# Performance work log

Hardware: AMD Instinct MI355X
Metric: run time of the kernel (lower is better)

Reference implementation:

```python
import jax, jax.numpy as jnp
import numpy as np

N_DRUG = 50000
N_GENE = 50000
E = 600000
D_IN = 128
D_HID = 64
D_EMB = 32


def setup_inputs() -> dict:
    key = jax.random.key(0)
    ks = jax.random.split(key, 32)
    inp = {}
    inp['x_drug'] = jax.random.normal(ks[0], (N_DRUG, D_IN), jnp.float32)
    inp['x_gene'] = jax.random.normal(ks[1], (N_GENE, D_IN), jnp.float32)
    # per-etype edge lists (src,dst)
    inp['dd_src'] = jax.random.randint(ks[2], (E,), 0, N_DRUG)
    inp['dd_dst'] = jax.random.randint(ks[3], (E,), 0, N_DRUG)
    inp['dg_src'] = jax.random.randint(ks[4], (E,), 0, N_DRUG)
    inp['dg_dst'] = jax.random.randint(ks[5], (E,), 0, N_GENE)
    inp['gd_src'] = jax.random.randint(ks[6], (E,), 0, N_GENE)
    inp['gd_dst'] = jax.random.randint(ks[7], (E,), 0, N_DRUG)
    inp['gg_src'] = jax.random.randint(ks[8], (E,), 0, N_GENE)
    inp['gg_dst'] = jax.random.randint(ks[9], (E,), 0, N_GENE)
    # layer-1 per-relation weights (in -> hidden) and per-ntype biases
    s1 = 1.0 / np.sqrt(D_IN)
    inp['W1_dd'] = jax.random.normal(ks[10], (D_IN, D_HID), jnp.float32) * s1
    inp['W1_dg'] = jax.random.normal(ks[11], (D_IN, D_HID), jnp.float32) * s1
    inp['W1_gd'] = jax.random.normal(ks[12], (D_IN, D_HID), jnp.float32) * s1
    inp['W1_gg'] = jax.random.normal(ks[13], (D_IN, D_HID), jnp.float32) * s1
    inp['b1_drug'] = jnp.zeros((D_HID,), jnp.float32)
    inp['b1_gene'] = jnp.zeros((D_HID,), jnp.float32)
    # layer-2 per-relation weights (hidden -> embed) and per-ntype biases
    s2 = 1.0 / np.sqrt(D_HID)
    inp['W2_dd'] = jax.random.normal(ks[14], (D_HID, D_EMB), jnp.float32) * s2
    inp['W2_dg'] = jax.random.normal(ks[15], (D_HID, D_EMB), jnp.float32) * s2
    inp['W2_gd'] = jax.random.normal(ks[16], (D_HID, D_EMB), jnp.float32) * s2
    inp['W2_gg'] = jax.random.normal(ks[17], (D_HID, D_EMB), jnp.float32) * s2
    inp['b2_drug'] = jnp.zeros((D_EMB,), jnp.float32)
    inp['b2_gene'] = jnp.zeros((D_EMB,), jnp.float32)
    return inp


def _rel_mean(x_src, W, src, dst, n_dst):
    # transform-then-gather (efficient when out_dim <= in_dim), segment-mean over dst
    m = (x_src @ W)[src]                                  # [E, out]
    s = jax.ops.segment_sum(m, dst, num_segments=n_dst)   # [n_dst, out]
    deg = jax.ops.segment_sum(jnp.ones((src.shape[0],), m.dtype), dst, num_segments=n_dst)
    return s / jnp.maximum(deg, 1.0)[:, None]


def _rgcn_layer(xd, xg, Wdd, Wdg, Wgd, Wgg, bd, bg,
                dd_src, dd_dst, dg_src, dg_dst, gd_src, gd_dst, gg_src, gg_dst, act):
    hd = (_rel_mean(xd, Wdd, dd_src, dd_dst, N_DRUG)
          + _rel_mean(xg, Wgd, gd_src, gd_dst, N_DRUG) + bd)
    hg = (_rel_mean(xd, Wdg, dg_src, dg_dst, N_GENE)
          + _rel_mean(xg, Wgg, gg_src, gg_dst, N_GENE) + bg)
    if act:
        hd = jax.nn.relu(hd)
        hg = jax.nn.relu(hg)
    return hd, hg


def reference(x_drug, x_gene, dd_src, dd_dst, dg_src, dg_dst, gd_src, gd_dst,
              gg_src, gg_dst, W1_dd, W1_dg, W1_gd, W1_gg, b1_drug, b1_gene,
              W2_dd, W2_dg, W2_gd, W2_gg, b2_drug, b2_gene):
    hd, hg = _rgcn_layer(x_drug, x_gene, W1_dd, W1_dg, W1_gd, W1_gg, b1_drug, b1_gene,
                         dd_src, dd_dst, dg_src, dg_dst, gd_src, gd_dst, gg_src, gg_dst, True)
    hd, hg = _rgcn_layer(hd, hg, W2_dd, W2_dg, W2_gd, W2_gg, b2_drug, b2_gene,
                         dd_src, dd_dst, dg_src, dg_dst, gd_src, gd_dst, gg_src, gg_dst, False)
    # concatenate per-ntype embeddings: rows [0:N_DRUG]=drug, [N_DRUG:]=gene
    return jnp.concatenate([hd, hg], axis=0)
```

## Files before the change

### kernel.cpp

```cpp
#include <hip/hip_runtime.h>
#include <hip/hip_bf16.h>

#define N_NODE 50000
#define NEDGE  600000
#define NRANGE 128
#define RSZ    391
#define CAPB   6144
#define CHUNK  4096
#define NBLK1  147

typedef __hip_bfloat16 bf16;
struct __attribute__((aligned(8))) bh4 { bf16 a, b, c, d; };
typedef __attribute__((ext_vector_type(8))) short short8;
typedef __attribute__((ext_vector_type(4))) float floatx4;

__device__ __forceinline__ short f2s(float f) {
    bf16 t = __float2bfloat16(f);
    return *(short*)&t;
}


__global__ __launch_bounds__(256) void k_part(
    const int* __restrict__ d0, const int* __restrict__ s0,
    const int* __restrict__ d1, const int* __restrict__ s1,
    const int* __restrict__ d2, const int* __restrict__ s2,
    const int* __restrict__ d3, const int* __restrict__ s3,
    int* __restrict__ gcur, unsigned* __restrict__ gpart)
{
    __shared__ int hcur[NRANGE];
    __shared__ int delta[NRANGE];
    __shared__ int sc[256];
    __shared__ unsigned buf[CHUNK];
    int bid = blockIdx.x;
    int rel = bid / NBLK1;
    int c   = bid - rel * NBLK1;
    int tid = threadIdx.x;
    const int* dp = rel == 0 ? d0 : rel == 1 ? d1 : rel == 2 ? d2 : d3;
    const int* sp = rel == 0 ? s0 : rel == 1 ? s1 : rel == 2 ? s2 : s3;
    int e0 = c * CHUNK;
    int e1 = min(e0 + CHUNK, NEDGE);
    int cnt_chunk = e1 - e0;

    if (tid < NRANGE) hcur[tid] = 0;
    __syncthreads();
    for (int e = e0 + tid; e < e1; e += 256)
        atomicAdd(&hcur[dp[e] / RSZ], 1);
    __syncthreads();
    int v = (tid < NRANGE) ? hcur[tid] : 0;
    sc[tid] = v;
    __syncthreads();
    for (int d = 1; d < NRANGE; d <<= 1) {
        int t = (tid >= d && tid < NRANGE) ? sc[tid - d] : 0;
        __syncthreads();
        sc[tid] += t;
        __syncthreads();
    }
    if (tid < NRANGE) {
        int start = sc[tid] - v;
        int bg    = rel * NRANGE + tid;
        int resv  = atomicAdd(&gcur[bg], v);
        delta[tid] = bg * CAPB + resv - start;
        hcur[tid]  = start;
    }
    __syncthreads();
    for (int e = e0 + tid; e < e1; e += 256) {
        int d = dp[e];
        int b = d / RSZ;
        int p = atomicAdd(&hcur[b], 1);
        buf[p] = ((unsigned)b << 25) | ((unsigned)(d - b * RSZ) << 16) | (unsigned)sp[e];
    }
    __syncthreads();
    for (int i = tid; i < cnt_chunk; i += 256) {
        unsigned key = buf[i];
        gpart[delta[key >> 25] + i] = key;
    }
}

__global__ __launch_bounds__(512) void k_base(
    const int* __restrict__ gcur, int* __restrict__ base_rel)
{
    __shared__ int sc[512];
    int t = threadIdx.x;
    int v = gcur[t];
    sc[t] = v;
    __syncthreads();
    int loc = t & (NRANGE - 1);
    for (int d = 1; d < NRANGE; d <<= 1) {
        int x = (loc >= d) ? sc[t - d] : 0;
        __syncthreads();
        sc[t] += x;
        __syncthreads();
    }
    base_rel[t] = sc[t] - v;
}

__global__ __launch_bounds__(256) void k_csr(
    const unsigned* __restrict__ gpart, const int* __restrict__ gcnt,
    const int* __restrict__ base_rel, int* __restrict__ off, int* __restrict__ edges)
{
    __shared__ int cur[RSZ];
    __shared__ unsigned short stg[CAPB];
    __shared__ int sc[256];
    int bid = blockIdx.x;
    int rel = bid >> 7, r = bid & (NRANGE - 1);
    int tid = threadIdx.x;
    int range0 = r * RSZ;
    int RS = min(RSZ, N_NODE - range0);
    if (RS < 0) RS = 0;
    int count = gcnt[bid];
    int base  = base_rel[bid];
    size_t slot0 = (size_t)bid * CAPB;

    for (int i = tid; i < RSZ; i += 256) cur[i] = 0;
    __syncthreads();
    for (int i = tid; i < count; i += 256)
        atomicAdd(&cur[(gpart[slot0 + i] >> 16) & 0x1FF], 1);
    __syncthreads();
    int vloc[2]; int run = 0;
#pragma unroll
    for (int j = 0; j < 2; j++) {
        int idx = tid * 2 + j;
        int x = (idx < RSZ) ? cur[idx] : 0;
        vloc[j] = x; run += x;
    }
    sc[tid] = run;
    __syncthreads();
    for (int d = 1; d < 256; d <<= 1) {
        int t = (tid >= d) ? sc[tid - d] : 0;
        __syncthreads();
        sc[tid] += t;
        __syncthreads();
    }
    int excl = sc[tid] - run;
    run = excl;
#pragma unroll
    for (int j = 0; j < 2; j++) {
        int idx = tid * 2 + j;
        if (idx < RSZ) { int x = vloc[j]; cur[idx] = run; run += x; }
    }
    __syncthreads();
    for (int i = tid; i < RS; i += 256)
        off[rel * (N_NODE + 1) + range0 + i] = base + cur[i];
    if (r == NRANGE - 1 && tid == 0) off[rel * (N_NODE + 1) + N_NODE] = NEDGE;
    __syncthreads();
    for (int i = tid; i < count; i += 256) {
        unsigned key = gpart[slot0 + i];
        int p = atomicAdd(&cur[(key >> 16) & 0x1FF], 1);
        stg[p] = (unsigned short)(key & 0xFFFFu);
    }
    __syncthreads();
    for (int i = tid; i < count; i += 256)
        edges[rel * NEDGE + base + i] = (int)stg[i];
}

template <int K, int NOUT, bool AFP32>
__global__ __launch_bounds__(256) void k_gemm_pair(
    const void* __restrict__ X0, const void* __restrict__ X1,
    const float* __restrict__ Wa0, const float* __restrict__ Wb0,
    const float* __restrict__ Wa1, const float* __restrict__ Wb1,
    bf16* __restrict__ out0, bf16* __restrict__ out1, int M)
{
    constexpr int NB  = NOUT / 16;
    constexpr int KC  = K / 32;
    constexpr int NH  = NOUT / 2;
    constexpr int NBL = (NB == 8) ? 3 : 2;
    __shared__ short Wl[KC * NB * 512];

    int sel = blockIdx.y;
    const void*  X  = sel ? X1 : X0;
    const float* Wa = sel ? Wa1 : Wa0;
    const float* Wb = sel ? Wb1 : Wb0;
    bf16*        out = sel ? out1 : out0;

    int tid = threadIdx.x;
    for (int i = tid; i < KC * NB * 512; i += 256) {
        int j  = i & 7;
        int n  = (i >> 3) & 15;
        int q  = (i >> 7) & 3;
        int nb = (i >> 9) & (NB - 1);
        int kc = i >> (9 + NBL);
        int k  = kc * 32 + q * 8 + j;
        int c  = nb * 16 + n;
        float w = (c < NH) ? Wa[k * NH + c] : Wb[k * NH + (c - NH)];
        Wl[i] = f2s(w);
    }
    __syncthreads();

    int lane = tid & 63, wv = tid >> 6;
    int q = lane >> 4, lidx = lane & 15;
    int row0 = blockIdx.x * 64 + wv * 16;
    int rowA = min(row0 + lidx, M - 1);

    floatx4 acc[NB];
#pragma unroll
    for (int nb = 0; nb < NB; nb++) acc[nb] = (floatx4){0.f, 0.f, 0.f, 0.f};

#pragma unroll
    for (int kc = 0; kc < KC; kc++) {
        short8 a;
        if constexpr (AFP32) {
            const float* Xf = (const float*)X + (size_t)rowA * K + kc * 32 + q * 8;
            float4 f0 = *(const float4*)Xf;
            float4 f1 = *(const float4*)(Xf + 4);
            a[0] = f2s(f0.x); a[1] = f2s(f0.y); a[2] = f2s(f0.z); a[3] = f2s(f0.w);
            a[4] = f2s(f1.x); a[5] = f2s(f1.y); a[6] = f2s(f1.z); a[7] = f2s(f1.w);
        } else {
            a = *(const short8*)((const short*)X + (size_t)rowA * K + kc * 32 + q * 8);
        }
#pragma unroll
        for (int nb = 0; nb < NB; nb++) {
            short8 b = *(const short8*)&Wl[((kc * NB + nb) * 64 + lane) * 8];
            acc[nb] = __builtin_amdgcn_mfma_f32_16x16x32_bf16(a, b, acc[nb], 0, 0, 0);
        }
    }
#pragma unroll
    for (int nb = 0; nb < NB; nb++) {
#pragma unroll
        for (int r = 0; r < 4; r++) {
            int row = row0 + q * 4 + r;
            if (row < M)
                out[(size_t)row * NOUT + nb * 16 + lidx] = __float2bfloat16(acc[nb][r]);
        }
    }
}

__device__ __forceinline__ void seg_sum64u(
    const unsigned short* __restrict__ mb, int ldm,
    int beg, int end, const int* __restrict__ edges,
    int lane, int lgrp, const unsigned short* base, float s[4])
{
    for (int e = beg; e < end; e += 64) {
        int nb = min(64, end - e);
        int eidx = (lane < nb) ? edges[e + lane] : 0;
        int full = nb & ~7;
        int j = 0;
        for (; j < full; j += 8) {
            int sa = __shfl(eidx, j + lgrp);
            int sb = __shfl(eidx, j + 4 + lgrp);
            uint2 wa = *(const uint2*)(base + (size_t)sa * ldm);
            uint2 wb = *(const uint2*)(base + (size_t)sb * ldm);
            s[0] += __uint_as_float(wa.x << 16);
            s[1] += __uint_as_float(wa.x & 0xFFFF0000u);
            s[2] += __uint_as_float(wa.y << 16);
            s[3] += __uint_as_float(wa.y & 0xFFFF0000u);
            s[0] += __uint_as_float(wb.x << 16);
            s[1] += __uint_as_float(wb.x & 0xFFFF0000u);
            s[2] += __uint_as_float(wb.y << 16);
            s[3] += __uint_as_float(wb.y & 0xFFFF0000u);
        }
        for (; j < nb; j += 4) {
            int sa = __shfl(eidx, j + lgrp);
            float vm = (j + lgrp < nb) ? 1.f : 0.f;
            uint2 w = *(const uint2*)(base + (size_t)sa * ldm);
            s[0] += vm * __uint_as_float(w.x << 16);
            s[1] += vm * __uint_as_float(w.x & 0xFFFF0000u);
            s[2] += vm * __uint_as_float(w.y << 16);
            s[3] += vm * __uint_as_float(w.y & 0xFFFF0000u);
        }
    }
}

__global__ __launch_bounds__(256) void k_gather64x2(
    const bf16* __restrict__ m1, const bf16* __restrict__ m2,
    const int* __restrict__ offA0, const int* __restrict__ eA0,
    const int* __restrict__ offB0, const int* __restrict__ eB0,
    const float* __restrict__ bias0, bf16* __restrict__ out0,
    const int* __restrict__ offA1, const int* __restrict__ eA1,
    const int* __restrict__ offB1, const int* __restrict__ eB1,
    const float* __restrict__ bias1, bf16* __restrict__ out1)
{
    int gw   = (blockIdx.x * 256 + threadIdx.x) >> 6;
    int lane = threadIdx.x & 63;
    int half = (gw >= N_NODE);
    int wid  = gw - (half ? N_NODE : 0);
    const int* offA = half ? offA1 : offA0;
    const int* eA   = half ? eA1   : eA0;
    const int* offB = half ? offB1 : offB0;
    const int* eB   = half ? eB1   : eB0;
    const float* bias = half ? bias1 : bias0;
    bf16* out = half ? out1 : out0;
    int col = half ? 64 : 0;

    int lgrp = lane >> 4, lidx = lane & 15;
    const unsigned short* mb1 = (const unsigned short*)m1;
    const unsigned short* mb2 = (const unsigned short*)m2;
    const unsigned short* base1 = mb1 + col + lidx * 4;
    const unsigned short* base2 = mb2 + col + lidx * 4;

    int begA = offA[wid], endA = offA[wid + 1];
    int begB = offB[wid], endB = offB[wid + 1];
    float sA[4] = {0.f, 0.f, 0.f, 0.f}, sB[4] = {0.f, 0.f, 0.f, 0.f};
    seg_sum64u(mb1, 128, begA, endA, eA, lane, lgrp, base1, sA);
    seg_sum64u(mb2, 128, begB, endB, eB, lane, lgrp, base2, sB);
#pragma unroll
    for (int k = 0; k < 4; k++) {
        sA[k] += __shfl_xor(sA[k], 16); sA[k] += __shfl_xor(sA[k], 32);
        sB[k] += __shfl_xor(sB[k], 16); sB[k] += __shfl_xor(sB[k], 32);
    }
    if (lane < 16) {
        float ia = 1.f / (float)max(endA - begA, 1);
        float ib = 1.f / (float)max(endB - begB, 1);
        float h0 = fmaxf(sA[0] * ia + sB[0] * ib + bias[lidx * 4 + 0], 0.f);
        float h1 = fmaxf(sA[1] * ia + sB[1] * ib + bias[lidx * 4 + 1], 0.f);
        float h2 = fmaxf(sA[2] * ia + sB[2] * ib + bias[lidx * 4 + 2], 0.f);
        float h3 = fmaxf(sA[3] * ia + sB[3] * ib + bias[lidx * 4 + 3], 0.f);
        bh4 v = { __float2bfloat16(h0), __float2bfloat16(h1),
                  __float2bfloat16(h2), __float2bfloat16(h3) };
        *(bh4*)(out + (size_t)wid * 64 + lidx * 4) = v;
    }
}

__device__ __forceinline__ void seg_sum32u(
    int beg, int end, const int* __restrict__ edges,
    int lane, int lgrp, int ldm, const unsigned short* base, float s[4])
{
    for (int e = beg; e < end; e += 64) {
        int nb = min(64, end - e);
        int eidx = (lane < nb) ? edges[e + lane] : 0;
        int full = nb & ~15;
        int j = 0;
        for (; j < full; j += 16) {
            int sa = __shfl(eidx, j + lgrp);
            int sb = __shfl(eidx, j + 8 + lgrp);
            uint2 wa = *(const uint2*)(base + (size_t)sa * ldm);
            uint2 wb = *(const uint2*)(base + (size_t)sb * ldm);
            s[0] += __uint_as_float(wa.x << 16);
            s[1] += __uint_as_float(wa.x & 0xFFFF0000u);
            s[2] += __uint_as_float(wa.y << 16);
            s[3] += __uint_as_float(wa.y & 0xFFFF0000u);
            s[0] += __uint_as_float(wb.x << 16);
            s[1] += __uint_as_float(wb.x & 0xFFFF0000u);
            s[2] += __uint_as_float(wb.y << 16);
            s[3] += __uint_as_float(wb.y & 0xFFFF0000u);
        }
        for (; j < nb; j += 8) {
            int sa = __shfl(eidx, j + lgrp);
            float vm = (j + lgrp < nb) ? 1.f : 0.f;
            uint2 w = *(const uint2*)(base + (size_t)sa * ldm);
            s[0] += vm * __uint_as_float(w.x << 16);
            s[1] += vm * __uint_as_float(w.x & 0xFFFF0000u);
            s[2] += vm * __uint_as_float(w.y << 16);
            s[3] += vm * __uint_as_float(w.y & 0xFFFF0000u);
        }
    }
}

__global__ __launch_bounds__(256) void k_gather32x2(
    const bf16* __restrict__ m1, const bf16* __restrict__ m2,
    const int* __restrict__ offA0, const int* __restrict__ eA0,
    const int* __restrict__ offB0, const int* __restrict__ eB0,
    const float* __restrict__ bias0, float* __restrict__ out0,
    const int* __restrict__ offA1, const int* __restrict__ eA1,
    const int* __restrict__ offB1, const int* __restrict__ eB1,
    const float* __restrict__ bias1, float* __restrict__ out1)
{
    int gw   = (blockIdx.x * 256 + threadIdx.x) >> 6;
    int lane = threadIdx.x & 63;
    int half = (gw >= N_NODE);
    int wid  = gw - (half ? N_NODE : 0);
    const int* offA = half ? offA1 : offA0;
    const int* eA   = half ? eA1   : eA0;
    const int* offB = half ? offB1 : offB0;
    const int* eB   = half ? eB1   : eB0;
    const float* bias = half ? bias1 : bias0;
    float* out = half ? out1 : out0;
    int col = half ? 32 : 0;

    int lgrp = lane >> 3, lidx = lane & 7;
    const unsigned short* base1 = (const unsigned short*)m1 + col + lidx * 4;
    const unsigned short* base2 = (const unsigned short*)m2 + col + lidx * 4;

    int begA = offA[wid], endA = offA[wid + 1];
    int begB = offB[wid], endB = offB[wid + 1];
    float sA[4] = {0.f, 0.f, 0.f, 0.f}, sB[4] = {0.f, 0.f, 0.f, 0.f};
    seg_sum32u(begA, endA, eA, lane, lgrp, 64, base1, sA);
    seg_sum32u(begB, endB, eB, lane, lgrp, 64, base2, sB);
#pragma unroll
    for (int k = 0; k < 4; k++) {
        sA[k] += __shfl_xor(sA[k], 8); sA[k] += __shfl_xor(sA[k], 16); sA[k] += __shfl_xor(sA[k], 32);
        sB[k] += __shfl_xor(sB[k], 8); sB[k] += __shfl_xor(sB[k], 16); sB[k] += __shfl_xor(sB[k], 32);
    }
    if (lane < 8) {
        float ia = 1.f / (float)max(endA - begA, 1);
        float ib = 1.f / (float)max(endB - begB, 1);
        float4 v;
        v.x = sA[0] * ia + sB[0] * ib + bias[lidx * 4 + 0];
        v.y = sA[1] * ia + sB[1] * ib + bias[lidx * 4 + 1];
        v.z = sA[2] * ia + sB[2] * ib + bias[lidx * 4 + 2];
        v.w = sA[3] * ia + sB[3] * ib + bias[lidx * 4 + 3];
        *(float4*)(out + (size_t)wid * 32 + lidx * 4) = v;
    }
}

extern "C" void kernel_launch(void* const* d_in, const int* in_sizes, int n_in,
                              void* d_out, int out_size, void* d_ws, size_t ws_size,
                              hipStream_t stream)
{
    const float* xd = (const float*)d_in[0];
    const float* xg = (const float*)d_in[1];
    const int* dd_src = (const int*)d_in[2];  const int* dd_dst = (const int*)d_in[3];
    const int* dg_src = (const int*)d_in[4];  const int* dg_dst = (const int*)d_in[5];
    const int* gd_src = (const int*)d_in[6];  const int* gd_dst = (const int*)d_in[7];
    const int* gg_src = (const int*)d_in[8];  const int* gg_dst = (const int*)d_in[9];
    const float* W1dd = (const float*)d_in[10];
    const float* W1dg = (const float*)d_in[11];
    const float* W1gd = (const float*)d_in[12];
    const float* W1gg = (const float*)d_in[13];
    const float* b1d  = (const float*)d_in[14];
    const float* b1g  = (const float*)d_in[15];
    const float* W2dd = (const float*)d_in[16];
    const float* W2dg = (const float*)d_in[17];
    const float* W2gd = (const float*)d_in[18];
    const float* W2gg = (const float*)d_in[19];
    const float* b2d  = (const float*)d_in[20];
    const float* b2g  = (const float*)d_in[21];
    float* out = (float*)d_out;

    int* gcur     = (int*)d_ws;
    int* base_rel = gcur + 512;
    int* off      = base_rel + 512;
    int* edges    = off + 4 * (N_NODE + 1);
    bf16* md1     = (bf16*)(edges + 4 * NEDGE);
    bf16* mg1     = md1 + (size_t)N_NODE * 128;
    bf16* hd      = mg1 + (size_t)N_NODE * 128;
    bf16* hg      = hd + (size_t)N_NODE * 64;
    bf16* md2     = md1;
    bf16* mg2     = mg1;
    unsigned* gpart = (unsigned*)md1;

    hipMemsetAsync(gcur, 0, 512 * sizeof(int), stream);
    k_part<<<4 * NBLK1, 256, 0, stream>>>(
        dd_dst, dd_src, gd_dst, gd_src, dg_dst, dg_src, gg_dst, gg_src, gcur, gpart);
    k_base<<<1, 512, 0, stream>>>(gcur, base_rel);
    k_csr<<<512, 256, 0, stream>>>(gpart, gcur, base_rel, off, edges);

    const int* off_dd = off + 0 * (N_NODE + 1);
    const int* off_gd = off + 1 * (N_NODE + 1);
    const int* off_dg = off + 2 * (N_NODE + 1);
    const int* off_gg = off + 3 * (N_NODE + 1);
    const int* e_dd = edges + 0 * NEDGE;
    const int* e_gd = edges + 1 * NEDGE;
    const int* e_dg = edges + 2 * NEDGE;
    const int* e_gg = edges + 3 * NEDGE;

    dim3 gemm_grid((N_NODE + 63) / 64, 2);
    int gather_grid = 2 * N_NODE / 4;

    k_gemm_pair<128, 128, true><<<gemm_grid, 256, 0, stream>>>(
        xd, xg, W1dd, W1dg, W1gd, W1gg, md1, mg1, N_NODE);
    k_gather64x2<<<gather_grid, 256, 0, stream>>>(
        md1, mg1,
        off_dd, e_dd, off_gd, e_gd, b1d, hd,
        off_dg, e_dg, off_gg, e_gg, b1g, hg);

    k_gemm_pair<64, 64, false><<<gemm_grid, 256, 0, stream>>>(
        hd, hg, W2dd, W2dg, W2gd, W2gg, md2, mg2, N_NODE);
    k_gather32x2<<<gather_grid, 256, 0, stream>>>(
        md2, mg2,
        off_dd, e_dd, off_gd, e_gd, b2d, out,
        off_dg, e_dg, off_gg, e_gg, b2g, out + (size_t)N_NODE * 32);
}
```

Measured before the change: 357.6 us.

## Split gathers into per-relation column-sliced tasks with separate combine kernels

Replaces each fused two-relation gather kernel with a task kernel that processes one relation and one 32-column slice per block. Partial means go to a workspace buffer, and a separate elementwise combine kernel adds bias and applies ReLU. Blocks are interleaved by task index so the gathered rows for a given relation and slice stay cache-resident, which is meant to improve locality of the random gathers. In exchange it adds two extra launches and writes and rereads the intermediate partials, with bf16 rounding of the layer-1 partials before they are summed.

```diff
diff --git a/kernel.cpp b/kernel.cpp
--- a/kernel.cpp
+++ b/kernel.cpp
@@ -8,6 +8,7 @@
 #define CAPB   6144
 #define CHUNK  4096
 #define NBLK1  147
+#define SP1    (N_NODE * 32)
 
 typedef __hip_bfloat16 bf16;
 struct __attribute__((aligned(8))) bh4 { bf16 a, b, c, d; };
@@ -224,172 +225,172 @@
     }
 }
 
-__device__ __forceinline__ void seg_sum64u(
-    const unsigned short* __restrict__ mb, int ldm,
-    int beg, int end, const int* __restrict__ edges,
-    int lane, int lgrp, const unsigned short* base, float s[4])
-{
+__global__ __launch_bounds__(256) void k_gtask1(
+    const bf16* __restrict__ md1, const bf16* __restrict__ mg1,
+    const int* __restrict__ off, const int* __restrict__ edges,
+    bf16* __restrict__ p1)
+{
+    int b = blockIdx.x;
+    int t = b & 7;
+    int wv = threadIdx.x >> 6, lane = threadIdx.x & 63;
+    int node = (b >> 3) * 4 + wv;
+    if (node >= N_NODE) return;
+    int r = t >> 1, c = t & 1;
+    const bf16* M = (r == 0 || r == 2) ? md1 : mg1;
+    int col0 = (r < 2 ? 0 : 64) + c * 32;
+    const int* offr = off + r * (N_NODE + 1);
+    const int* er   = edges + r * NEDGE;
+    int beg = offr[node], end = offr[node + 1];
+    int lgrp = lane >> 3, lidx = lane & 7;
+    const unsigned* base = (const unsigned*)M + (col0 >> 1) + lidx * 2;
+    float s0 = 0.f, s1 = 0.f, s2 = 0.f, s3 = 0.f;
     for (int e = beg; e < end; e += 64) {
         int nb = min(64, end - e);
-        int eidx = (lane < nb) ? edges[e + lane] : 0;
-        int full = nb & ~7;
-        int j = 0;
-        for (; j < full; j += 8) {
-            int sa = __shfl(eidx, j + lgrp);
-            int sb = __shfl(eidx, j + 4 + lgrp);
-            uint2 wa = *(const uint2*)(base + (size_t)sa * ldm);
-            uint2 wb = *(const uint2*)(base + (size_t)sb * ldm);
-            s[0] += __uint_as_float(wa.x << 16);
-            s[1] += __uint_as_float(wa.x & 0xFFFF0000u);
-            s[2] += __uint_as_float(wa.y << 16);
-            s[3] += __uint_as_float(wa.y & 0xFFFF0000u);
-            s[0] += __uint_as_float(wb.x << 16);
-            s[1] += __uint_as_float(wb.x & 0xFFFF0000u);
-            s[2] += __uint_as_float(wb.y << 16);
-            s[3] += __uint_as_float(wb.y & 0xFFFF0000u);
-        }
-        for (; j < nb; j += 4) {
-            int sa = __shfl(eidx, j + lgrp);
-            float vm = (j + lgrp < nb) ? 1.f : 0.f;
-            uint2 w = *(const uint2*)(base + (size_t)sa * ldm);
-            s[0] += vm * __uint_as_float(w.x << 16);
-            s[1] += vm * __uint_as_float(w.x & 0xFFFF0000u);
-            s[2] += vm * __uint_as_float(w.y << 16);
-            s[3] += vm * __uint_as_float(w.y & 0xFFFF0000u);
-        }
-    }
-}
-
-__global__ __launch_bounds__(256) void k_gather64x2(
-    const bf16* __restrict__ m1, const bf16* __restrict__ m2,
-    const int* __restrict__ offA0, const int* __restrict__ eA0,
-    const int* __restrict__ offB0, const int* __restrict__ eB0,
-    const float* __restrict__ bias0, bf16* __restrict__ out0,
-    const int* __restrict__ offA1, const int* __restrict__ eA1,
-    const int* __restrict__ offB1, const int* __restrict__ eB1,
-    const float* __restrict__ bias1, bf16* __restrict__ out1)
-{
-    int gw   = (blockIdx.x * 256 + threadIdx.x) >> 6;
-    int lane = threadIdx.x & 63;
-    int half = (gw >= N_NODE);
-    int wid  = gw - (half ? N_NODE : 0);
-    const int* offA = half ? offA1 : offA0;
-    const int* eA   = half ? eA1   : eA0;
-    const int* offB = half ? offB1 : offB0;
-    const int* eB   = half ? eB1   : eB0;
-    const float* bias = half ? bias1 : bias0;
-    bf16* out = half ? out1 : out0;
-    int col = half ? 64 : 0;
-
-    int lgrp = lane >> 4, lidx = lane & 15;
-    const unsigned short* mb1 = (const unsigned short*)m1;
-    const unsigned short* mb2 = (const unsigned short*)m2;
-    const unsigned short* base1 = mb1 + col + lidx * 4;
-    const unsigned short* base2 = mb2 + col + lidx * 4;
-
-    int begA = offA[wid], endA = offA[wid + 1];
-    int begB = offB[wid], endB = offB[wid + 1];
-    float sA[4] = {0.f, 0.f, 0.f, 0.f}, sB[4] = {0.f, 0.f, 0.f, 0.f};
-    seg_sum64u(mb1, 128, begA, endA, eA, lane, lgrp, base1, sA);
-    seg_sum64u(mb2, 128, begB, endB, eB, lane, lgrp, base2, sB);
-#pragma unroll
-    for (int k = 0; k < 4; k++) {
-        sA[k] += __shfl_xor(sA[k], 16); sA[k] += __shfl_xor(sA[k], 32);
-        sB[k] += __shfl_xor(sB[k], 16); sB[k] += __shfl_xor(sB[k], 32);
-    }
-    if (lane < 16) {
-        float ia = 1.f / (float)max(endA - begA, 1);
-        float ib = 1.f / (float)max(endB - begB, 1);
-        float h0 = fmaxf(sA[0] * ia + sB[0] * ib + bias[lidx * 4 + 0], 0.f);
-        float h1 = fmaxf(sA[1] * ia + sB[1] * ib + bias[lidx * 4 + 1], 0.f);
-        float h2 = fmaxf(sA[2] * ia + sB[2] * ib + bias[lidx * 4 + 2], 0.f);
-        float h3 = fmaxf(sA[3] * ia + sB[3] * ib + bias[lidx * 4 + 3], 0.f);
-        bh4 v = { __float2bfloat16(h0), __float2bfloat16(h1),
-                  __float2bfloat16(h2), __float2bfloat16(h3) };
-        *(bh4*)(out + (size_t)wid * 64 + lidx * 4) = v;
-    }
-}
-
-__device__ __forceinline__ void seg_sum32u(
-    int beg, int end, const int* __restrict__ edges,
-    int lane, int lgrp, int ldm, const unsigned short* base, float s[4])
-{
-    for (int e = beg; e < end; e += 64) {
-        int nb = min(64, end - e);
-        int eidx = (lane < nb) ? edges[e + lane] : 0;
+        int eidx = (lane < nb) ? er[e + lane] : 0;
         int full = nb & ~15;
         int j = 0;
         for (; j < full; j += 16) {
             int sa = __shfl(eidx, j + lgrp);
             int sb = __shfl(eidx, j + 8 + lgrp);
-            uint2 wa = *(const uint2*)(base + (size_t)sa * ldm);
-            uint2 wb = *(const uint2*)(base + (size_t)sb * ldm);
-            s[0] += __uint_as_float(wa.x << 16);
-            s[1] += __uint_as_float(wa.x & 0xFFFF0000u);
-            s[2] += __uint_as_float(wa.y << 16);
-            s[3] += __uint_as_float(wa.y & 0xFFFF0000u);
-            s[0] += __uint_as_float(wb.x << 16);
-            s[1] += __uint_as_float(wb.x & 0xFFFF0000u);
-            s[2] += __uint_as_float(wb.y << 16);
-            s[3] += __uint_as_float(wb.y & 0xFFFF0000u);
+            uint2 wa = *(const uint2*)(base + (size_t)sa * 64);
+            uint2 wb = *(const uint2*)(base + (size_t)sb * 64);
+            s0 += __uint_as_float(wa.x << 16);
+            s1 += __uint_as_float(wa.x & 0xFFFF0000u);
+            s2 += __uint_as_float(wa.y << 16);
+            s3 += __uint_as_float(wa.y & 0xFFFF0000u);
+            s0 += __uint_as_float(wb.x << 16);
+            s1 += __uint_as_float(wb.x & 0xFFFF0000u);
+            s2 += __uint_as_float(wb.y << 16);
+            s3 += __uint_as_float(wb.y & 0xFFFF0000u);
         }
         for (; j < nb; j += 8) {
             int sa = __shfl(eidx, j + lgrp);
             float vm = (j + lgrp < nb) ? 1.f : 0.f;
-            uint2 w = *(const uint2*)(base + (size_t)sa * ldm);
-            s[0] += vm * __uint_as_float(w.x << 16);
-            s[1] += vm * __uint_as_float(w.x & 0xFFFF0000u);
-            s[2] += vm * __uint_as_float(w.y << 16);
-            s[3] += vm * __uint_as_float(w.y & 0xFFFF0000u);
-        }
-    }
-}
-
-__global__ __launch_bounds__(256) void k_gather32x2(
-    const bf16* __restrict__ m1, const bf16* __restrict__ m2,
-    const int* __restrict__ offA0, const int* __restrict__ eA0,
-    const int* __restrict__ offB0, const int* __restrict__ eB0,
-    const float* __restrict__ bias0, float* __restrict__ out0,
-    const int* __restrict__ offA1, const int* __restrict__ eA1,
-    const int* __restrict__ offB1, const int* __restrict__ eB1,
-    const float* __restrict__ bias1, float* __restrict__ out1)
-{
-    int gw   = (blockIdx.x * 256 + threadIdx.x) >> 6;
-    int lane = threadIdx.x & 63;
-    int half = (gw >= N_NODE);
-    int wid  = gw - (half ? N_NODE : 0);
-    const int* offA = half ? offA1 : offA0;
-    const int* eA   = half ? eA1   : eA0;
-    const int* offB = half ? offB1 : offB0;
-    const int* eB   = half ? eB1   : eB0;
-    const float* bias = half ? bias1 : bias0;
-    float* out = half ? out1 : out0;
-    int col = half ? 32 : 0;
-
+            uint2 w = *(const uint2*)(base + (size_t)sa * 64);
+            s0 += vm * __uint_as_float(w.x << 16);
+            s1 += vm * __uint_as_float(w.x & 0xFFFF0000u);
+            s2 += vm * __uint_as_float(w.y << 16);
+            s3 += vm * __uint_as_float(w.y & 0xFFFF0000u);
+        }
+    }
+    s0 += __shfl_xor(s0, 8); s0 += __shfl_xor(s0, 16); s0 += __shfl_xor(s0, 32);
+    s1 += __shfl_xor(s1, 8); s1 += __shfl_xor(s1, 16); s1 += __shfl_xor(s1, 32);
+    s2 += __shfl_xor(s2, 8); s2 += __shfl_xor(s2, 16); s2 += __shfl_xor(s2, 32);
+    s3 += __shfl_xor(s3, 8); s3 += __shfl_xor(s3, 16); s3 += __shfl_xor(s3, 32);
+    if (lane < 8) {
+        float inv = 1.f / (float)max(end - beg, 1);
+        bh4 v = { __float2bfloat16(s0 * inv), __float2bfloat16(s1 * inv),
+                  __float2bfloat16(s2 * inv), __float2bfloat16(s3 * inv) };
+        *(bh4*)(p1 + (size_t)t * SP1 + (size_t)node * 32 + lidx * 4) = v;
+    }
+}
+
+__global__ __launch_bounds__(256) void k_combine1(
+    const bf16* __restrict__ p1, const float* __restrict__ b1d,
+    const float* __restrict__ b1g, bf16* __restrict__ hd, bf16* __restrict__ hg)
+{
+    int id = blockIdx.x * 256 + threadIdx.x;
+    if (id >= 2 * N_NODE * 16) return;
+    int half = id >= N_NODE * 16;
+    int rem = id - half * N_NODE * 16;
+    int n = rem >> 4, u = rem & 15;
+    int f0 = u * 4, ch = u >> 3, fi = f0 & 31;
+    const unsigned short* pa = (const unsigned short*)p1
+        + ((size_t)((half ? 4 : 0) + ch)) * SP1 + (size_t)n * 32 + fi;
+    const unsigned short* pb = (const unsigned short*)p1
+        + ((size_t)((half ? 6 : 2) + ch)) * SP1 + (size_t)n * 32 + fi;
+    uint2 wa = *(const uint2*)pa;
+    uint2 wb = *(const uint2*)pb;
+    const float* bias = (half ? b1g : b1d) + f0;
+    float h0 = fmaxf(__uint_as_float(wa.x << 16)          + __uint_as_float(wb.x << 16)          + bias[0], 0.f);
+    float h1 = fmaxf(__uint_as_float(wa.x & 0xFFFF0000u)  + __uint_as_float(wb.x & 0xFFFF0000u)  + bias[1], 0.f);
+    float h2 = fmaxf(__uint_as_float(wa.y << 16)          + __uint_as_float(wb.y << 16)          + bias[2], 0.f);
+    float h3 = fmaxf(__uint_as_float(wa.y & 0xFFFF0000u)  + __uint_as_float(wb.y & 0xFFFF0000u)  + bias[3], 0.f);
+    bf16* h = half ? hg : hd;
+    bh4 v = { __float2bfloat16(h0), __float2bfloat16(h1),
+              __float2bfloat16(h2), __float2bfloat16(h3) };
+    *(bh4*)(h + (size_t)n * 64 + f0) = v;
+}
+
+__global__ __launch_bounds__(256) void k_gtask2(
+    const bf16* __restrict__ md2, const bf16* __restrict__ mg2,
+    const int* __restrict__ off, const int* __restrict__ edges,
+    float* __restrict__ p2)
+{
+    int b = blockIdx.x;
+    int t = b & 7;
+    int wv = threadIdx.x >> 6, lane = threadIdx.x & 63;
+    int r = t >> 1, nh = t & 1;
+    int node = nh * (N_NODE / 2) + (b >> 3) * 4 + wv;
+    int nend = nh * (N_NODE / 2) + N_NODE / 2;
+    if (node >= nend) return;
+    const bf16* M = (r == 0 || r == 2) ? md2 : mg2;
+    int col0 = (r < 2) ? 0 : 32;
+    const int* offr = off + r * (N_NODE + 1);
+    const int* er   = edges + r * NEDGE;
+    int beg = offr[node], end = offr[node + 1];
     int lgrp = lane >> 3, lidx = lane & 7;
-    const unsigned short* base1 = (const unsigned short*)m1 + col + lidx * 4;
-    const unsigned short* base2 = (const unsigned short*)m2 + col + lidx * 4;
-
-    int begA = offA[wid], endA = offA[wid + 1];
-    int begB = offB[wid], endB = offB[wid + 1];
-    float sA[4] = {0.f, 0.f, 0.f, 0.f}, sB[4] = {0.f, 0.f, 0.f, 0.f};
-    seg_sum32u(begA, endA, eA, lane, lgrp, 64, base1, sA);
-    seg_sum32u(begB, endB, eB, lane, lgrp, 64, base2, sB);
-#pragma unroll
-    for (int k = 0; k < 4; k++) {
-        sA[k] += __shfl_xor(sA[k], 8); sA[k] += __shfl_xor(sA[k], 16); sA[k] += __shfl_xor(sA[k], 32);
-        sB[k] += __shfl_xor(sB[k], 8); sB[k] += __shfl_xor(sB[k], 16); sB[k] += __shfl_xor(sB[k], 32);
-    }
+    const unsigned* base = (const unsigned*)M + (col0 >> 1) + lidx * 2;
+    float s0 = 0.f, s1 = 0.f, s2 = 0.f, s3 = 0.f;
+    for (int e = beg; e < end; e += 64) {
+        int nb = min(64, end - e);
+        int eidx = (lane < nb) ? er[e + lane] : 0;
+        int full = nb & ~15;
+        int j = 0;
+        for (; j < full; j += 16) {
+            int sa = __shfl(eidx, j + lgrp);
+            int sb = __shfl(eidx, j + 8 + lgrp);
+            uint2 wa = *(const uint2*)(base + (size_t)sa * 32);
+            uint2 wb = *(const uint2*)(base + (size_t)sb * 32);
+            s0 += __uint_as_float(wa.x << 16);
+            s1 += __uint_as_float(wa.x & 0xFFFF0000u);
+            s2 += __uint_as_float(wa.y << 16);
+            s3 += __uint_as_float(wa.y & 0xFFFF0000u);
+            s0 += __uint_as_float(wb.x << 16);
+            s1 += __uint_as_float(wb.x & 0xFFFF0000u);
+            s2 += __uint_as_float(wb.y << 16);
+            s3 += __uint_as_float(wb.y & 0xFFFF0000u);
+        }
+        for (; j < nb; j += 8) {
+            int sa = __shfl(eidx, j + lgrp);
+            float vm = (j + lgrp < nb) ? 1.f : 0.f;
+            uint2 w = *(const uint2*)(base + (size_t)sa * 32);
+            s0 += vm * __uint_as_float(w.x << 16);
+            s1 += vm * __uint_as_float(w.x & 0xFFFF0000u);
+            s2 += vm * __uint_as_float(w.y << 16);
+            s3 += vm * __uint_as_float(w.y & 0xFFFF0000u);
+        }
+    }
+    s0 += __shfl_xor(s0, 8); s0 += __shfl_xor(s0, 16); s0 += __shfl_xor(s0, 32);
+    s1 += __shfl_xor(s1, 8); s1 += __shfl_xor(s1, 16); s1 += __shfl_xor(s1, 32);
+    s2 += __shfl_xor(s2, 8); s2 += __shfl_xor(s2, 16); s2 += __shfl_xor(s2, 32);
+    s3 += __shfl_xor(s3, 8); s3 += __shfl_xor(s3, 16); s3 += __shfl_xor(s3, 32);
     if (lane < 8) {
-        float ia = 1.f / (float)max(endA - begA, 1);
-        float ib = 1.f / (float)max(endB - begB, 1);
-        float4 v;
-        v.x = sA[0] * ia + sB[0] * ib + bias[lidx * 4 + 0];
-        v.y = sA[1] * ia + sB[1] * ib + bias[lidx * 4 + 1];
-        v.z = sA[2] * ia + sB[2] * ib + bias[lidx * 4 + 2];
-        v.w = sA[3] * ia + sB[3] * ib + bias[lidx * 4 + 3];
-        *(float4*)(out + (size_t)wid * 32 + lidx * 4) = v;
-    }
+        float inv = 1.f / (float)max(end - beg, 1);
+        float4 v = make_float4(s0 * inv, s1 * inv, s2 * inv, s3 * inv);
+        *(float4*)(p2 + (size_t)r * SP1 + (size_t)node * 32 + lidx * 4) = v;
+    }
+}
+
+__global__ __launch_bounds__(256) void k_combine2(
+    const float* __restrict__ p2, const float* __restrict__ b2d,
+    const float* __restrict__ b2g, float* __restrict__ out)
+{
+    int id = blockIdx.x * 256 + threadIdx.x;
+    if (id >= 2 * N_NODE * 8) return;
+    int half = id >= N_NODE * 8;
+    int rem = id - half * N_NODE * 8;
+    int n = rem >> 3, u = rem & 7;
+    int f0 = u * 4;
+    const float* pa = p2 + (size_t)(half ? 2 : 0) * SP1 + (size_t)n * 32 + f0;
+    const float* pb = p2 + (size_t)(half ? 3 : 1) * SP1 + (size_t)n * 32 + f0;
+    float4 va = *(const float4*)pa;
+    float4 vb = *(const float4*)pb;
+    const float* bias = (half ? b2g : b2d) + f0;
+    float4 o = make_float4(va.x + vb.x + bias[0], va.y + vb.y + bias[1],
+                           va.z + vb.z + bias[2], va.w + vb.w + bias[3]);
+    size_t row = (half ? N_NODE : 0) + n;
+    *(float4*)(out + row * 32 + f0) = o;
 }
 
 extern "C" void kernel_launch(void* const* d_in, const int* in_sizes, int n_in,
@@ -422,7 +423,9 @@
     int* edges    = off + 4 * (N_NODE + 1);
     bf16* md1     = (bf16*)(edges + 4 * NEDGE);
     bf16* mg1     = md1 + (size_t)N_NODE * 128;
-    bf16* hd      = mg1 + (size_t)N_NODE * 128;
+    bf16* p1      = mg1 + (size_t)N_NODE * 128;
+    float* p2     = (float*)p1;
+    bf16* hd      = p1 + 8 * (size_t)SP1;
     bf16* hg      = hd + (size_t)N_NODE * 64;
     bf16* md2     = md1;
     bf16* mg2     = mg1;
@@ -434,29 +437,15 @@
     k_base<<<1, 512, 0, stream>>>(gcur, base_rel);
     k_csr<<<512, 256, 0, stream>>>(gpart, gcur, base_rel, off, edges);
 
-    const int* off_dd = off + 0 * (N_NODE + 1);
-    const int* off_gd = off + 1 * (N_NODE + 1);
-    const int* off_dg = off + 2 * (N_NODE + 1);
-    const int* off_gg = off + 3 * (N_NODE + 1);
-    const int* e_dd = edges + 0 * NEDGE;
-    const int* e_gd = edges + 1 * NEDGE;
-    const int* e_dg = edges + 2 * NEDGE;
-    const int* e_gg = edges + 3 * NEDGE;
-
     dim3 gemm_grid((N_NODE + 63) / 64, 2);
-    int gather_grid = 2 * N_NODE / 4;
 
     k_gemm_pair<128, 128, true><<<gemm_grid, 256, 0, stream>>>(
         xd, xg, W1dd, W1dg, W1gd, W1gg, md1, mg1, N_NODE);
-    k_gather64x2<<<gather_grid, 256, 0, stream>>>(
-        md1, mg1,
-        off_dd, e_dd, off_gd, e_gd, b1d, hd,
-        off_dg, e_dg, off_gg, e_gg, b1g, hg);
+    k_gtask1<<<8 * (N_NODE / 4), 256, 0, stream>>>(md1, mg1, off, edges, p1);
+    k_combine1<<<(2 * N_NODE * 16) / 256, 256, 0, stream>>>(p1, b1d, b1g, hd, hg);
 
     k_gemm_pair<64, 64, false><<<gemm_grid, 256, 0, stream>>>(
         hd, hg, W2dd, W2dg, W2gd, W2gg, md2, mg2, N_NODE);
-    k_gather32x2<<<gather_grid, 256, 0, stream>>>(
-        md2, mg2,
-        off_dd, e_dd, off_gd, e_gd, b2d, out,
-        off_dg, e_dg, off_gg, e_gg, b2g, out + (size_t)N_NODE * 32);
-}
+    k_gtask2<<<8 * (N_NODE / 8), 256, 0, stream>>>(md2, mg2, off, edges, p2);
+    k_combine2<<<(2 * N_NODE * 8) / 256, 256, 0, stream>>>(p2, b2d, b2g, out);
+}
```

After: 411.6 us. +15.1%, slower.
